# Optimization experiments

Measured on AMD Instinct MI355X. Metric: run time of the kernel, lower is better.

The kernel has to match this reference:

```python
import jax, jax.numpy as jnp
import numpy as np

B, L, D, H, U = 1024, 256, 256, 512, 512


def setup_inputs() -> dict:
    key = jax.random.key(0)
    ks = jax.random.split(key, 5)
    scale_f = 1.0
    return {
        "features": jax.random.normal(ks[0], (B, L, D), dtype=jnp.float32),
        "hidden": jax.random.normal(ks[1], (B, H), dtype=jnp.float32),
        "W1": jax.random.normal(ks[2], (D, U), dtype=jnp.float32) / np.sqrt(D),
        "b1": jnp.zeros((U,), dtype=jnp.float32),
        "W2": jax.random.normal(ks[3], (H, U), dtype=jnp.float32) / np.sqrt(H),
        "b2": jnp.zeros((U,), dtype=jnp.float32),
        "Wv": jax.random.normal(ks[4], (U, 1), dtype=jnp.float32) / np.sqrt(U),
        "bv": jnp.zeros((1,), dtype=jnp.float32),
    }


def reference(features, hidden, W1, b1, W2, b2, Wv, bv):
    # features: [B, L, D], hidden: [B, H]
    proj_f = jnp.einsum("bld,du->blu", features, W1) + b1      # [B, L, U]
    proj_h = (hidden @ W2 + b2)[:, None, :]                      # [B, 1, U]
    score = jnp.tanh(proj_f + proj_h)                            # [B, L, U]
    logits = jnp.einsum("blu,uo->blo", score, Wv) + bv           # [B, L, 1]
    attention_weights = jax.nn.softmax(logits, axis=1)           # [B, L, 1]
    context_vector = jnp.sum(attention_weights * features, axis=1)  # [B, D]
    return (context_vector, attention_weights)
```

## Files before the change

kernel.cpp:

```cpp
#include <hip/hip_runtime.h>
#include <hip/hip_bf16.h>

#define B_ 1024
#define L_ 256
#define D_ 256
#define H_ 512
#define U_ 512
#define M_ (B_ * L_)

#define BM 128
#define BN 128
#define BK 64

typedef float f32x4 __attribute__((ext_vector_type(4)));
typedef short bf16x8 __attribute__((ext_vector_type(8)));

__device__ __forceinline__ short f2bf(float f) {
  unsigned u = __float_as_uint(f);
  u += 0x7fffu + ((u >> 16) & 1u);
  return (short)(u >> 16);
}

__device__ __forceinline__ void load16_g2l(const void* g, void* l) {
  __builtin_amdgcn_global_load_lds(
      (const __attribute__((address_space(1))) unsigned int*)g,
      (__attribute__((address_space(3))) unsigned int*)l, 16, 0, 0);
}

__device__ __forceinline__ float fast_tanh(float x) {
  float e = __expf(2.0f * x);
  return 1.0f - 2.0f * __builtin_amdgcn_rcpf(e + 1.0f);
}

__global__ void k_w1t(const float* __restrict__ W1, short* __restrict__ W1T) {
  int idx = blockIdx.x * 256 + threadIdx.x;
  int u = idx >> 8;
  int d = idx & 255;
  W1T[idx] = f2bf(W1[(size_t)d * U_ + u]);
}

__global__ void k_projh(const float* __restrict__ hidden, const float* __restrict__ W2,
                        const float* __restrict__ b1, const float* __restrict__ b2,
                        float* __restrict__ ph) {
  int u = blockIdx.x * 256 + threadIdx.x;
  int b0 = blockIdx.y * 8;
  float acc[8] = {0.f, 0.f, 0.f, 0.f, 0.f, 0.f, 0.f, 0.f};
  for (int h = 0; h < H_; ++h) {
    float w = W2[(size_t)h * U_ + u];
#pragma unroll
    for (int i = 0; i < 8; ++i) acc[i] = fmaf(hidden[(size_t)(b0 + i) * H_ + h], w, acc[i]);
  }
  float bias = b1[u] + b2[u];
#pragma unroll
  for (int i = 0; i < 8; ++i) ph[(size_t)(b0 + i) * U_ + u] = acc[i] + bias;
}

__global__ __launch_bounds__(256, 3) void k_gemm(
    const float* __restrict__ F,
    const short* __restrict__ W1T,
    const float* __restrict__ ph,
    const float* __restrict__ Wv,
    float* __restrict__ logits) {
  __shared__ __align__(16) short As[BM * BK];
  __shared__ __align__(16) short Bs[BN * BK];

  const int tid = threadIdx.x;
  const int lane = tid & 63;
  const int hi = lane >> 4;
  const int wid = tid >> 6;
  const int wr = wid >> 1, wc = wid & 1;
  const int tile = ((blockIdx.x & 7) << 10) | (blockIdx.x >> 3);
  const int ntile = tile & 3;
  const int mtile = tile >> 2;
  const int m0 = mtile * BM;
  const int n0 = ntile * BN;
  const int b = m0 >> 8;

  const bf16x8* As8 = (const bf16x8*)As;
  const bf16x8* Bs8 = (const bf16x8*)Bs;

  const float* agp[4];
  int aslot[4];
  const short* bgp[4];
#pragma unroll
  for (int i = 0; i < 4; ++i) {
    int s = i * 256 + tid;
    int arow = s >> 3;
    int akq = (s & 7) ^ (arow & 7);
    agp[i] = F + (size_t)(m0 + arow) * D_ + akq * 8;
    aslot[i] = s;
    bgp[i] = W1T + (size_t)(n0 + arow) * D_ + akq * 8;
  }

  f32x4 acc[4][4];
  const f32x4 fz = {0.f, 0.f, 0.f, 0.f};
#pragma unroll
  for (int mi = 0; mi < 4; ++mi)
#pragma unroll
    for (int ni = 0; ni < 4; ++ni) acc[mi][ni] = fz;

  for (int kt = 0; kt < 4; ++kt) {
    f32x4 ar[4][2];
#pragma unroll
    for (int i = 0; i < 4; ++i) {
      ar[i][0] = *(const f32x4*)(agp[i]);
      ar[i][1] = *(const f32x4*)(agp[i] + 4);
      agp[i] += BK;
    }
    if (kt) __syncthreads();
#pragma unroll
    for (int i = 0; i < 4; ++i) {
      load16_g2l(bgp[i], &Bs[(size_t)(i * 256 + tid) * 8]);
      bgp[i] += BK;
    }
#pragma unroll
    for (int i = 0; i < 4; ++i) {
      bf16x8 w;
#pragma unroll
      for (int j = 0; j < 4; ++j) { w[j] = f2bf(ar[i][0][j]); w[4 + j] = f2bf(ar[i][1][j]); }
      ((bf16x8*)As)[aslot[i]] = w;
    }
    __syncthreads();

#pragma unroll
    for (int kk = 0; kk < 2; ++kk) {
      bf16x8 af[4], bfr[4];
#pragma unroll
      for (int mi = 0; mi < 4; ++mi) {
        int rA = wr * 64 + mi * 16 + (lane & 15);
        af[mi] = As8[rA * 8 + ((kk * 4 + hi) ^ (rA & 7))];
      }
#pragma unroll
      for (int ni = 0; ni < 4; ++ni) {
        int nB = wc * 64 + ni * 16 + (lane & 15);
        bfr[ni] = Bs8[nB * 8 + ((kk * 4 + hi) ^ (nB & 7))];
      }
#pragma unroll
      for (int mi = 0; mi < 4; ++mi)
#pragma unroll
        for (int ni = 0; ni < 4; ++ni)
          acc[mi][ni] = __builtin_amdgcn_mfma_f32_16x16x32_bf16(af[mi], bfr[ni], acc[mi][ni], 0, 0, 0);
    }
  }

  const float* phr = ph + (size_t)b * U_;
  float phv[4], wvv[4];
#pragma unroll
  for (int ni = 0; ni < 4; ++ni) {
    int u = n0 + wc * 64 + ni * 16 + (lane & 15);
    phv[ni] = phr[u];
    wvv[ni] = Wv[u];
  }
#pragma unroll
  for (int mi = 0; mi < 4; ++mi) {
    float cs[4] = {0.f, 0.f, 0.f, 0.f};
#pragma unroll
    for (int ni = 0; ni < 4; ++ni) {
#pragma unroll
      for (int r = 0; r < 4; ++r) {
        float x = acc[mi][ni][r] + phv[ni];
        cs[r] += fast_tanh(x) * wvv[ni];
      }
    }
#pragma unroll
    for (int off = 1; off < 16; off <<= 1) {
#pragma unroll
      for (int r = 0; r < 4; ++r) cs[r] += __shfl_xor(cs[r], off);
    }
    if ((lane & 15) == 0) {
      int g = m0 + wr * 64 + mi * 16 + ((lane >> 4) << 2);
#pragma unroll
      for (int r = 0; r < 4; ++r) atomicAdd(&logits[g + r], cs[r]);
    }
  }
}

__global__ void k_smctx(const float* __restrict__ logits, const float* __restrict__ F,
                        float* __restrict__ outw, float* __restrict__ ctx) {
  __shared__ float wl[L_];
  __shared__ f32x4 part[256];
  __shared__ float red[8];
  int b = blockIdx.x, t = threadIdx.x;
  float x = logits[(size_t)b * L_ + t];
  float m = x;
#pragma unroll
  for (int off = 32; off >= 1; off >>= 1) m = fmaxf(m, __shfl_xor(m, off));
  if ((t & 63) == 0) red[t >> 6] = m;
  __syncthreads();
  m = fmaxf(fmaxf(red[0], red[1]), fmaxf(red[2], red[3]));
  float e = __expf(x - m);
  float s = e;
#pragma unroll
  for (int off = 32; off >= 1; off >>= 1) s += __shfl_xor(s, off);
  if ((t & 63) == 0) red[4 + (t >> 6)] = s;
  __syncthreads();
  s = (red[4] + red[5]) + (red[6] + red[7]);
  float w = e / s;
  outw[(size_t)b * L_ + t] = w;
  wl[t] = w;
  __syncthreads();

  int lq = t >> 6, dq = t & 63;
  const f32x4* F4 = (const f32x4*)(F + (size_t)b * L_ * D_);
  f32x4 acc = {0.f, 0.f, 0.f, 0.f};
  for (int l = lq; l < L_; l += 4) acc += wl[l] * F4[l * 64 + dq];
  part[t] = acc;
  __syncthreads();
  if (lq == 0) {
    f32x4 r = (part[t] + part[t + 64]) + (part[t + 128] + part[t + 192]);
    ((f32x4*)ctx)[(size_t)b * 64 + dq] = r;
  }
}

extern "C" void kernel_launch(void* const* d_in, const int* in_sizes, int n_in,
                              void* d_out, int out_size, void* d_ws, size_t ws_size,
                              hipStream_t stream) {
  const float* F      = (const float*)d_in[0];
  const float* hidden = (const float*)d_in[1];
  const float* W1     = (const float*)d_in[2];
  const float* b1     = (const float*)d_in[3];
  const float* W2     = (const float*)d_in[4];
  const float* b2     = (const float*)d_in[5];
  const float* Wv     = (const float*)d_in[6];

  float* out_ctx = (float*)d_out;
  float* out_w   = out_ctx + (size_t)B_ * D_;

  char* ws = (char*)d_ws;
  short* W1T   = (short*)ws;
  float* ph    = (float*)(ws + 262144);
  float* logits = (float*)(ws + 262144 + 2097152);

  hipMemsetAsync(logits, 0, (size_t)M_ * sizeof(float), stream);
  k_w1t<<<512, 256, 0, stream>>>(W1, W1T);
  k_projh<<<dim3(2, 128), 256, 0, stream>>>(hidden, W2, b1, b2, ph);
  k_gemm<<<8192, 256, 0, stream>>>(F, W1T, ph, Wv, logits);
  k_smctx<<<1024, 256, 0, stream>>>(logits, F, out_w, out_ctx);
}
```

Measured before the change: 240.5 us.

## Double-buffer GEMM tiles with smaller BN/BK and register prefetch

Shrinks the GEMM tile to 128x64 with K-step 32, and double-buffers LDS so the next K-slice of features and W1T is fetched while MFMAs run on the current one, with a single barrier per step. The grid doubles and occupancy is raised to 4 blocks per CU. In exchange, each features row tile is loaded and converted to bf16 twice as often, and there are twice as many atomic adds into the logits.

```diff
diff --git a/kernel.cpp b/kernel.cpp
--- a/kernel.cpp
+++ b/kernel.cpp
@@ -9,8 +9,9 @@
 #define M_ (B_ * L_)
 
 #define BM 128
-#define BN 128
-#define BK 64
+#define BN 64
+#define BK 32
+#define NKT 8
 
 typedef float f32x4 __attribute__((ext_vector_type(4)));
 typedef short bf16x8 __attribute__((ext_vector_type(8)));
@@ -55,99 +56,114 @@
   for (int i = 0; i < 8; ++i) ph[(size_t)(b0 + i) * U_ + u] = acc[i] + bias;
 }
 
-__global__ __launch_bounds__(256, 3) void k_gemm(
+__global__ __launch_bounds__(256, 4) void k_gemm(
     const float* __restrict__ F,
     const short* __restrict__ W1T,
     const float* __restrict__ ph,
     const float* __restrict__ Wv,
     float* __restrict__ logits) {
-  __shared__ __align__(16) short As[BM * BK];
-  __shared__ __align__(16) short Bs[BN * BK];
+  __shared__ __align__(16) short As[2][BM * BK];
+  __shared__ __align__(16) short Bs[2][BN * BK];
 
   const int tid = threadIdx.x;
   const int lane = tid & 63;
   const int hi = lane >> 4;
   const int wid = tid >> 6;
   const int wr = wid >> 1, wc = wid & 1;
-  const int tile = ((blockIdx.x & 7) << 10) | (blockIdx.x >> 3);
-  const int ntile = tile & 3;
-  const int mtile = tile >> 2;
+  const int tile = ((blockIdx.x & 7) << 11) | (blockIdx.x >> 3);
+  const int ntile = tile & 7;
+  const int mtile = tile >> 3;
   const int m0 = mtile * BM;
   const int n0 = ntile * BN;
   const int b = m0 >> 8;
 
-  const bf16x8* As8 = (const bf16x8*)As;
-  const bf16x8* Bs8 = (const bf16x8*)Bs;
-
-  const float* agp[4];
-  int aslot[4];
-  const short* bgp[4];
-#pragma unroll
-  for (int i = 0; i < 4; ++i) {
-    int s = i * 256 + tid;
-    int arow = s >> 3;
-    int akq = (s & 7) ^ (arow & 7);
-    agp[i] = F + (size_t)(m0 + arow) * D_ + akq * 8;
-    aslot[i] = s;
-    bgp[i] = W1T + (size_t)(n0 + arow) * D_ + akq * 8;
-  }
-
-  f32x4 acc[4][4];
+  const float* agp0;
+  const float* agp1;
+  {
+    int s0 = tid, s1 = 256 + tid;
+    int r0 = s0 >> 2, r1 = s1 >> 2;
+    int c0 = ((s0 & 3) - (r0 >> 2)) & 3;
+    int c1 = ((s1 & 3) - (r1 >> 2)) & 3;
+    agp0 = F + (size_t)(m0 + r0) * D_ + c0 * 8;
+    agp1 = F + (size_t)(m0 + r1) * D_ + c1 * 8;
+  }
+  const short* bgp;
+  {
+    int n = tid >> 2;
+    int c = ((tid & 3) - (n >> 2)) & 3;
+    bgp = W1T + (size_t)(n0 + n) * D_ + c * 8;
+  }
+
+  f32x4 acc[4][2];
   const f32x4 fz = {0.f, 0.f, 0.f, 0.f};
 #pragma unroll
-  for (int mi = 0; mi < 4; ++mi)
-#pragma unroll
-    for (int ni = 0; ni < 4; ++ni) acc[mi][ni] = fz;
-
-  for (int kt = 0; kt < 4; ++kt) {
-    f32x4 ar[4][2];
-#pragma unroll
-    for (int i = 0; i < 4; ++i) {
-      ar[i][0] = *(const f32x4*)(agp[i]);
-      ar[i][1] = *(const f32x4*)(agp[i] + 4);
-      agp[i] += BK;
-    }
-    if (kt) __syncthreads();
-#pragma unroll
-    for (int i = 0; i < 4; ++i) {
-      load16_g2l(bgp[i], &Bs[(size_t)(i * 256 + tid) * 8]);
-      bgp[i] += BK;
-    }
-#pragma unroll
-    for (int i = 0; i < 4; ++i) {
-      bf16x8 w;
-#pragma unroll
-      for (int j = 0; j < 4; ++j) { w[j] = f2bf(ar[i][0][j]); w[4 + j] = f2bf(ar[i][1][j]); }
-      ((bf16x8*)As)[aslot[i]] = w;
+  for (int mi = 0; mi < 4; ++mi) {
+    acc[mi][0] = fz;
+    acc[mi][1] = fz;
+  }
+
+  int aslotr[4], bslotr[2];
+#pragma unroll
+  for (int mi = 0; mi < 4; ++mi) {
+    int rA = wr * 64 + mi * 16 + (lane & 15);
+    aslotr[mi] = rA * 4 + ((hi + (rA >> 2)) & 3);
+  }
+#pragma unroll
+  for (int ni = 0; ni < 2; ++ni) {
+    int nB = wc * 32 + ni * 16 + (lane & 15);
+    bslotr[ni] = nB * 4 + ((hi + (nB >> 2)) & 3);
+  }
+
+  f32x4 a0a = *(const f32x4*)(agp0);
+  f32x4 a0b = *(const f32x4*)(agp0 + 4);
+  f32x4 a1a = *(const f32x4*)(agp1);
+  f32x4 a1b = *(const f32x4*)(agp1 + 4);
+  agp0 += BK; agp1 += BK;
+  load16_g2l(bgp, &Bs[0][(size_t)tid * 8]);
+  bgp += BK;
+
+  for (int kt = 0; kt < NKT; ++kt) {
+    {
+      bf16x8 w0, w1;
+#pragma unroll
+      for (int j = 0; j < 4; ++j) {
+        w0[j] = f2bf(a0a[j]); w0[4 + j] = f2bf(a0b[j]);
+        w1[j] = f2bf(a1a[j]); w1[4 + j] = f2bf(a1b[j]);
+      }
+      ((bf16x8*)As[kt & 1])[tid] = w0;
+      ((bf16x8*)As[kt & 1])[256 + tid] = w1;
     }
     __syncthreads();
 
-#pragma unroll
-    for (int kk = 0; kk < 2; ++kk) {
-      bf16x8 af[4], bfr[4];
-#pragma unroll
-      for (int mi = 0; mi < 4; ++mi) {
-        int rA = wr * 64 + mi * 16 + (lane & 15);
-        af[mi] = As8[rA * 8 + ((kk * 4 + hi) ^ (rA & 7))];
-      }
-#pragma unroll
-      for (int ni = 0; ni < 4; ++ni) {
-        int nB = wc * 64 + ni * 16 + (lane & 15);
-        bfr[ni] = Bs8[nB * 8 + ((kk * 4 + hi) ^ (nB & 7))];
-      }
-#pragma unroll
-      for (int mi = 0; mi < 4; ++mi)
-#pragma unroll
-        for (int ni = 0; ni < 4; ++ni)
-          acc[mi][ni] = __builtin_amdgcn_mfma_f32_16x16x32_bf16(af[mi], bfr[ni], acc[mi][ni], 0, 0, 0);
+    if (kt < NKT - 1) {
+      a0a = *(const f32x4*)(agp0);
+      a0b = *(const f32x4*)(agp0 + 4);
+      a1a = *(const f32x4*)(agp1);
+      a1b = *(const f32x4*)(agp1 + 4);
+      agp0 += BK; agp1 += BK;
+      load16_g2l(bgp, &Bs[(kt + 1) & 1][(size_t)tid * 8]);
+      bgp += BK;
+    }
+
+    bf16x8 af[4], bfr[2];
+    const bf16x8* As8 = (const bf16x8*)As[kt & 1];
+    const bf16x8* Bs8 = (const bf16x8*)Bs[kt & 1];
+#pragma unroll
+    for (int mi = 0; mi < 4; ++mi) af[mi] = As8[aslotr[mi]];
+    bfr[0] = Bs8[bslotr[0]];
+    bfr[1] = Bs8[bslotr[1]];
+#pragma unroll
+    for (int mi = 0; mi < 4; ++mi) {
+      acc[mi][0] = __builtin_amdgcn_mfma_f32_16x16x32_bf16(af[mi], bfr[0], acc[mi][0], 0, 0, 0);
+      acc[mi][1] = __builtin_amdgcn_mfma_f32_16x16x32_bf16(af[mi], bfr[1], acc[mi][1], 0, 0, 0);
     }
   }
 
   const float* phr = ph + (size_t)b * U_;
-  float phv[4], wvv[4];
-#pragma unroll
-  for (int ni = 0; ni < 4; ++ni) {
-    int u = n0 + wc * 64 + ni * 16 + (lane & 15);
+  float phv[2], wvv[2];
+#pragma unroll
+  for (int ni = 0; ni < 2; ++ni) {
+    int u = n0 + wc * 32 + ni * 16 + (lane & 15);
     phv[ni] = phr[u];
     wvv[ni] = Wv[u];
   }
@@ -155,7 +171,7 @@
   for (int mi = 0; mi < 4; ++mi) {
     float cs[4] = {0.f, 0.f, 0.f, 0.f};
 #pragma unroll
-    for (int ni = 0; ni < 4; ++ni) {
+    for (int ni = 0; ni < 2; ++ni) {
 #pragma unroll
       for (int r = 0; r < 4; ++r) {
         float x = acc[mi][ni][r] + phv[ni];
@@ -168,7 +184,7 @@
       for (int r = 0; r < 4; ++r) cs[r] += __shfl_xor(cs[r], off);
     }
     if ((lane & 15) == 0) {
-      int g = m0 + wr * 64 + mi * 16 + ((lane >> 4) << 2);
+      int g = m0 + wr * 64 + mi * 16 + hi * 4;
 #pragma unroll
       for (int r = 0; r < 4; ++r) atomicAdd(&logits[g + r], cs[r]);
     }
@@ -234,6 +250,6 @@
   hipMemsetAsync(logits, 0, (size_t)M_ * sizeof(float), stream);
   k_w1t<<<512, 256, 0, stream>>>(W1, W1T);
   k_projh<<<dim3(2, 128), 256, 0, stream>>>(hidden, W2, b1, b2, ph);
-  k_gemm<<<8192, 256, 0, stream>>>(F, W1T, ph, Wv, logits);
+  k_gemm<<<16384, 256, 0, stream>>>(F, W1T, ph, Wv, logits);
   k_smctx<<<1024, 256, 0, stream>>>(logits, F, out_w, out_ctx);
 }
```

New measurement: 317.9 us. +32.2%, slower.

## Keep full-K A tile in LDS, stream pre-swizzled W1 fragments from global

Applied to the files above, without the earlier changes.

Each block now loads its 128-row features tile for the whole K=256 into LDS once, converting it to bf16, and loops over all four N tiles. This removes the previous 4x re-reading and re-converting of features across N tiles, along with the atomic logits accumulation and the memset. W1 is pre-permuted into an MFMA fragment layout so that B operands are read straight from global/L2 into registers, with a one-step register prefetch. The tanh-dot partial sums are reduced through LDS and written with plain stores. In exchange the LDS footprint grows to 64KB and occupancy drops to 2 blocks per CU, and the B loads are now exposed to global memory latency.

```diff
diff --git a/kernel.cpp b/kernel.cpp
--- a/kernel.cpp
+++ b/kernel.cpp
@@ -9,11 +9,10 @@
 #define M_ (B_ * L_)
 
 #define BM 128
-#define BN 128
-#define BK 64
 
 typedef float f32x4 __attribute__((ext_vector_type(4)));
 typedef short bf16x8 __attribute__((ext_vector_type(8)));
+typedef short bf16x4 __attribute__((ext_vector_type(4)));
 
 __device__ __forceinline__ short f2bf(float f) {
   unsigned u = __float_as_uint(f);
@@ -21,22 +20,21 @@
   return (short)(u >> 16);
 }
 
-__device__ __forceinline__ void load16_g2l(const void* g, void* l) {
-  __builtin_amdgcn_global_load_lds(
-      (const __attribute__((address_space(1))) unsigned int*)g,
-      (__attribute__((address_space(3))) unsigned int*)l, 16, 0, 0);
-}
-
 __device__ __forceinline__ float fast_tanh(float x) {
   float e = __expf(2.0f * x);
   return 1.0f - 2.0f * __builtin_amdgcn_rcpf(e + 1.0f);
 }
 
-__global__ void k_w1t(const float* __restrict__ W1, short* __restrict__ W1T) {
-  int idx = blockIdx.x * 256 + threadIdx.x;
-  int u = idx >> 8;
-  int d = idx & 255;
-  W1T[idx] = f2bf(W1[(size_t)d * U_ + u]);
+__global__ void k_w1f(const float* __restrict__ W1, short* __restrict__ W1F) {
+  int i = blockIdx.x * 256 + threadIdx.x;
+  int jj = i & 7;
+  int no = (i >> 3) & 15;
+  int kc = (i >> 7) & 3;
+  int kb = (i >> 9) & 7;
+  int nb = i >> 12;
+  int u = nb * 16 + no;
+  int d = kb * 32 + kc * 8 + jj;
+  W1F[i] = f2bf(W1[(size_t)d * U_ + u]);
 }
 
 __global__ void k_projh(const float* __restrict__ hidden, const float* __restrict__ W2,
@@ -55,124 +53,124 @@
   for (int i = 0; i < 8; ++i) ph[(size_t)(b0 + i) * U_ + u] = acc[i] + bias;
 }
 
-__global__ __launch_bounds__(256, 3) void k_gemm(
+__global__ __launch_bounds__(256, 2) void k_gemm(
     const float* __restrict__ F,
-    const short* __restrict__ W1T,
+    const short* __restrict__ W1F,
     const float* __restrict__ ph,
     const float* __restrict__ Wv,
     float* __restrict__ logits) {
-  __shared__ __align__(16) short As[BM * BK];
-  __shared__ __align__(16) short Bs[BN * BK];
+  __shared__ __align__(16) short As[BM * D_];
+  __shared__ float csum[2][BM];
 
   const int tid = threadIdx.x;
   const int lane = tid & 63;
   const int hi = lane >> 4;
   const int wid = tid >> 6;
   const int wr = wid >> 1, wc = wid & 1;
-  const int tile = ((blockIdx.x & 7) << 10) | (blockIdx.x >> 3);
-  const int ntile = tile & 3;
-  const int mtile = tile >> 2;
-  const int m0 = mtile * BM;
-  const int n0 = ntile * BN;
+  const int m0 = blockIdx.x * BM;
   const int b = m0 >> 8;
 
-  const bf16x8* As8 = (const bf16x8*)As;
-  const bf16x8* Bs8 = (const bf16x8*)Bs;
-
-  const float* agp[4];
-  int aslot[4];
-  const short* bgp[4];
-#pragma unroll
-  for (int i = 0; i < 4; ++i) {
-    int s = i * 256 + tid;
-    int arow = s >> 3;
-    int akq = (s & 7) ^ (arow & 7);
-    agp[i] = F + (size_t)(m0 + arow) * D_ + akq * 8;
-    aslot[i] = s;
-    bgp[i] = W1T + (size_t)(n0 + arow) * D_ + akq * 8;
-  }
+  {
+    const float* sp = F + (size_t)(m0 + (tid >> 6)) * D_ + (tid & 63) * 4;
+    const int kq8 = (tid & 63) * 8;
+#pragma unroll
+    for (int jb = 0; jb < 2; ++jb) {
+      f32x4 sv[16];
+#pragma unroll
+      for (int j = 0; j < 16; ++j)
+        sv[j] = *(const f32x4*)(sp + (size_t)(jb * 16 + j) * 4 * D_);
+#pragma unroll
+      for (int j = 0; j < 16; ++j) {
+        int row = (jb * 16 + j) * 4 + (tid >> 6);
+        int boff = (row * 512 + kq8) ^ ((row & 7) << 4);
+        bf16x4 w;
+#pragma unroll
+        for (int q = 0; q < 4; ++q) w[q] = f2bf(sv[j][q]);
+        *(bf16x4*)((char*)As + boff) = w;
+      }
+    }
+  }
+  __syncthreads();
 
   f32x4 acc[4][4];
+  float cs[4][4];
   const f32x4 fz = {0.f, 0.f, 0.f, 0.f};
 #pragma unroll
   for (int mi = 0; mi < 4; ++mi)
 #pragma unroll
-    for (int ni = 0; ni < 4; ++ni) acc[mi][ni] = fz;
-
-  for (int kt = 0; kt < 4; ++kt) {
-    f32x4 ar[4][2];
-#pragma unroll
-    for (int i = 0; i < 4; ++i) {
-      ar[i][0] = *(const f32x4*)(agp[i]);
-      ar[i][1] = *(const f32x4*)(agp[i] + 4);
-      agp[i] += BK;
-    }
-    if (kt) __syncthreads();
-#pragma unroll
-    for (int i = 0; i < 4; ++i) {
-      load16_g2l(bgp[i], &Bs[(size_t)(i * 256 + tid) * 8]);
-      bgp[i] += BK;
-    }
-#pragma unroll
-    for (int i = 0; i < 4; ++i) {
-      bf16x8 w;
-#pragma unroll
-      for (int j = 0; j < 4; ++j) { w[j] = f2bf(ar[i][0][j]); w[4 + j] = f2bf(ar[i][1][j]); }
-      ((bf16x8*)As)[aslot[i]] = w;
-    }
-    __syncthreads();
-
-#pragma unroll
-    for (int kk = 0; kk < 2; ++kk) {
-      bf16x8 af[4], bfr[4];
+    for (int x = 0; x < 4; ++x) { acc[mi][x] = fz; cs[mi][x] = 0.f; }
+
+  const short* bbase = W1F + (size_t)(wc * 32) * 512 + lane * 8;
+  bf16x8 bcur[4], bnxt[4];
+#pragma unroll
+  for (int ni = 0; ni < 4; ++ni)
+    bcur[ni] = *(const bf16x8*)(bbase + (size_t)(ni * 8) * 512);
+
+  const float* phr = ph + (size_t)b * U_;
+  const int rbase = wr * 64 + (lane & 15);
+
+  for (int nt = 0; nt < 4; ++nt) {
+#pragma unroll
+    for (int kt = 0; kt < 8; ++kt) {
+      if (nt * 8 + kt < 31) {
+        const int ktn = (kt + 1) & 7;
+        const int ntn64 = (nt + ((kt + 1) >> 3)) * 64;
+#pragma unroll
+        for (int ni = 0; ni < 4; ++ni)
+          bnxt[ni] = *(const bf16x8*)(bbase + (size_t)(ntn64 + ni * 8 + ktn) * 512);
+      }
+      bf16x8 af[4];
 #pragma unroll
       for (int mi = 0; mi < 4; ++mi) {
-        int rA = wr * 64 + mi * 16 + (lane & 15);
-        af[mi] = As8[rA * 8 + ((kk * 4 + hi) ^ (rA & 7))];
-      }
-#pragma unroll
-      for (int ni = 0; ni < 4; ++ni) {
-        int nB = wc * 64 + ni * 16 + (lane & 15);
-        bfr[ni] = Bs8[nB * 8 + ((kk * 4 + hi) ^ (nB & 7))];
-      }
-#pragma unroll
-      for (int mi = 0; mi < 4; ++mi)
-#pragma unroll
-        for (int ni = 0; ni < 4; ++ni)
-          acc[mi][ni] = __builtin_amdgcn_mfma_f32_16x16x32_bf16(af[mi], bfr[ni], acc[mi][ni], 0, 0, 0);
-    }
-  }
-
-  const float* phr = ph + (size_t)b * U_;
-  float phv[4], wvv[4];
-#pragma unroll
-  for (int ni = 0; ni < 4; ++ni) {
-    int u = n0 + wc * 64 + ni * 16 + (lane & 15);
-    phv[ni] = phr[u];
-    wvv[ni] = Wv[u];
-  }
+        int rA = rbase + mi * 16;
+        int boff = (rA * 512 + kt * 64 + hi * 16) ^ ((rA & 7) << 4);
+        af[mi] = *(const bf16x8*)((const char*)As + boff);
+      }
+#pragma unroll
+      for (int mi = 0; mi < 4; ++mi) {
+        acc[mi][0] = __builtin_amdgcn_mfma_f32_16x16x32_bf16(af[mi], bcur[0], acc[mi][0], 0, 0, 0);
+        acc[mi][1] = __builtin_amdgcn_mfma_f32_16x16x32_bf16(af[mi], bcur[1], acc[mi][1], 0, 0, 0);
+        acc[mi][2] = __builtin_amdgcn_mfma_f32_16x16x32_bf16(af[mi], bcur[2], acc[mi][2], 0, 0, 0);
+        acc[mi][3] = __builtin_amdgcn_mfma_f32_16x16x32_bf16(af[mi], bcur[3], acc[mi][3], 0, 0, 0);
+      }
+#pragma unroll
+      for (int ni = 0; ni < 4; ++ni) bcur[ni] = bnxt[ni];
+    }
+#pragma unroll
+    for (int ni = 0; ni < 4; ++ni) {
+      int u = nt * 128 + wc * 64 + ni * 16 + (lane & 15);
+      float phv = phr[u];
+      float wvv = Wv[u];
+#pragma unroll
+      for (int mi = 0; mi < 4; ++mi) {
+#pragma unroll
+        for (int r = 0; r < 4; ++r) {
+          float x = acc[mi][ni][r] + phv;
+          cs[mi][r] += fast_tanh(x) * wvv;
+        }
+      }
+    }
+#pragma unroll
+    for (int mi = 0; mi < 4; ++mi)
+#pragma unroll
+      for (int x = 0; x < 4; ++x) acc[mi][x] = fz;
+  }
+
 #pragma unroll
   for (int mi = 0; mi < 4; ++mi) {
-    float cs[4] = {0.f, 0.f, 0.f, 0.f};
-#pragma unroll
-    for (int ni = 0; ni < 4; ++ni) {
-#pragma unroll
-      for (int r = 0; r < 4; ++r) {
-        float x = acc[mi][ni][r] + phv[ni];
-        cs[r] += fast_tanh(x) * wvv[ni];
-      }
-    }
 #pragma unroll
     for (int off = 1; off < 16; off <<= 1) {
 #pragma unroll
-      for (int r = 0; r < 4; ++r) cs[r] += __shfl_xor(cs[r], off);
+      for (int r = 0; r < 4; ++r) cs[mi][r] += __shfl_xor(cs[mi][r], off);
     }
     if ((lane & 15) == 0) {
-      int g = m0 + wr * 64 + mi * 16 + ((lane >> 4) << 2);
-#pragma unroll
-      for (int r = 0; r < 4; ++r) atomicAdd(&logits[g + r], cs[r]);
-    }
-  }
+      int rloc = wr * 64 + mi * 16 + hi * 4;
+#pragma unroll
+      for (int r = 0; r < 4; ++r) csum[wc][rloc + r] = cs[mi][r];
+    }
+  }
+  __syncthreads();
+  if (tid < BM) logits[m0 + tid] = csum[0][tid] + csum[1][tid];
 }
 
 __global__ void k_smctx(const float* __restrict__ logits, const float* __restrict__ F,
@@ -227,13 +225,12 @@
   float* out_w   = out_ctx + (size_t)B_ * D_;
 
   char* ws = (char*)d_ws;
-  short* W1T   = (short*)ws;
-  float* ph    = (float*)(ws + 262144);
+  short* W1F    = (short*)ws;
+  float* ph     = (float*)(ws + 262144);
   float* logits = (float*)(ws + 262144 + 2097152);
 
-  hipMemsetAsync(logits, 0, (size_t)M_ * sizeof(float), stream);
-  k_w1t<<<512, 256, 0, stream>>>(W1, W1T);
+  k_w1f<<<512, 256, 0, stream>>>(W1, W1F);
   k_projh<<<dim3(2, 128), 256, 0, stream>>>(hidden, W2, b1, b2, ph);
-  k_gemm<<<8192, 256, 0, stream>>>(F, W1T, ph, Wv, logits);
+  k_gemm<<<2048, 256, 0, stream>>>(F, W1F, ph, Wv, logits);
   k_smctx<<<1024, 256, 0, stream>>>(logits, F, out_w, out_ctx);
 }
```

Measured after the change: 254.8 us. 1.06x slower.
